# Kernel tuning notes

Hardware: AMD Instinct MI355X
Metric: run time of the kernel (lower is better)

The kernel has to match this reference:

```python
import jax, jax.numpy as jnp
import numpy as np


def rational_hat(points, centers, radius):
    # points: [B, P, 2], centers: [K, 2], radius: [1]
    # L1 distance of each point to each center: [B, P, K]
    norm = jnp.abs(points[:, :, None, :] - centers[None, None, :, :]).sum(-1)
    r = jnp.abs(radius[0])
    val = 1.0 / (1.0 + norm) - 1.0 / (1.0 + jnp.abs(r - norm))
    return val.sum(axis=1)  # [B, K]


def setup_inputs() -> dict:
    key = jax.random.key(0)
    k1, k2, k3, k4, k5 = jax.random.split(key, 5)
    B, N0, N1, N2, K = 32, 20000, 10000, 10000, 64
    return {
        "beta_0_up": jax.random.uniform(k1, (B, N0, 2), dtype=jnp.float32),
        "beta_0_down": jax.random.uniform(k2, (B, N0, 2), dtype=jnp.float32),
        "beta0_ext": jax.random.uniform(k3, (B, N1, 2), dtype=jnp.float32),
        "beta1_ext": jax.random.uniform(k4, (B, N2, 2), dtype=jnp.float32),
        "centers": jax.random.uniform(k5, (K, 2), dtype=jnp.float32),
        "radius": jnp.full((1,), 0.1, dtype=jnp.float32),
    }


def reference(beta_0_up, beta_0_down, beta0_ext, beta1_ext, centers, radius):
    x0, y0 = beta0_ext[..., 0], beta0_ext[..., 1]
    x1, y1 = beta1_ext[..., 0], beta1_ext[..., 1]
    b0_1st = jnp.stack([x0, 1.0 - x0], axis=-1)  # [B, N1, 2]
    b0_2nd = jnp.stack([y0, 1.0 - y0], axis=-1)
    b1_1st = jnp.stack([x1, 1.0 - x1], axis=-1)  # [B, N2, 2]
    b1_2nd = jnp.stack([y1, 1.0 - y1], axis=-1)
    ph_down = jnp.concatenate([beta_0_down, b0_1st, b1_1st], axis=1)  # [B, P, 2]
    ph_up = jnp.concatenate([beta_0_up, b0_2nd, b1_2nd], axis=1)
    up_out = rational_hat(ph_up, centers, radius)    # [B, K]
    down_out = rational_hat(ph_down, centers, radius)
    tpl = -((up_out - down_out) ** 2).sum()
    x = jnp.concatenate([up_out, down_out], axis=1)  # [B, 2K]
    return (x, tpl)
```

## Files before the change

kernel.cpp:

```cpp
#include <hip/hip_runtime.h>

#define NB 32
#define N0 20000
#define N1 10000
#define N2 10000
#define KC_A 8
#define KC_B 16
#define NBINS 4096
#define SENT 3.0e4f

__device__ __forceinline__ float sgpr(float x) {
    return __int_as_float(__builtin_amdgcn_readfirstlane(__float_as_int(x)));
}

__global__ __launch_bounds__(256, 8) void hat_kernel(
    const float* __restrict__ up0, const float* __restrict__ down0,
    const float* __restrict__ ext0, const float* __restrict__ ext1,
    const float* __restrict__ centers, const float* __restrict__ radius,
    float* __restrict__ out)
{
    const int tid  = threadIdx.x;
    const int lane = tid & 63;
    const int wave = tid >> 6;
    const float r  = sgpr(fabsf(radius[0]));
    const float nr = -r;

    __shared__ unsigned hist[NBINS];
    __shared__ float    red[4 * KC_B];

    if (blockIdx.x < 256) {
        const int id   = blockIdx.x;
        const int cc   = id & 3;
        const int side = (id >> 2) & 1;
        const int b    = id >> 3;
        const int cbase = cc * KC_B;

        for (int j = tid; j < NBINS; j += 256) hist[j] = 0;
        __syncthreads();

        const float2* e0 = (const float2*)(ext0 + (size_t)b * (N1*2));
        const float2* e1 = (const float2*)(ext1 + (size_t)b * (N2*2));
        for (int i = tid; i < N1; i += 256) {
            const float2 q0 = e0[i];
            const float2 q1 = e1[i];
            const float vv0 = (side == 0) ? q0.y : q0.x;
            const float vv1 = (side == 0) ? q1.y : q1.x;
            int b0 = (int)(vv0 * (float)NBINS);
            int b1 = (int)(vv1 * (float)NBINS);
            b0 = min(max(b0, 0), NBINS - 1);
            b1 = min(max(b1, 0), NBINS - 1);
            atomicAdd(&hist[b0], 1u);
            atomicAdd(&hist[b1], 1u);
        }
        __syncthreads();

        float Ak[KC_B], mk[KC_B];
        #pragma unroll
        for (int k = 0; k < KC_B; ++k) {
            const float cx = centers[2*(cbase+k)];
            const float cy = centers[2*(cbase+k)+1];
            Ak[k] = sgpr(fabsf(1.0f - (cx + cy)));
            mk[k] = sgpr(0.5f * (1.0f + (cx - cy)));
        }

        float part[KC_B];
        #pragma unroll
        for (int k = 0; k < KC_B; ++k) part[k] = 0.f;

        #pragma unroll
        for (int jj = 0; jj < NBINS/256; ++jj) {
            const int j = jj*256 + tid;
            const float cntf = (float)hist[j];
            const float vvj  = ((float)j + 0.5f) * (1.0f/(float)NBINS);
            #pragma unroll
            for (int k = 0; k < KC_B; ++k) {
                const float s  = vvj - mk[k];
                const float tt = fmaxf(Ak[k], 2.0f*fabsf(s));
                const float d1 = 1.0f + tt;
                const float rn = r - tt;
                const float d2 = 1.0f + fabsf(rn);
                const float rc = __builtin_amdgcn_rcpf(d1 * d2);
                part[k] = fmaf(cntf * (d2 - d1), rc, part[k]);
            }
        }

        {
            #pragma unroll
            for (int k = 0; k < 8; ++k) {
                const bool hi = lane & 32;
                const float send = hi ? part[k]   : part[k+8];
                const float keep = hi ? part[k+8] : part[k];
                part[k] = keep + __shfl_xor(send, 32, 64);
            }
            #pragma unroll
            for (int k = 0; k < 4; ++k) {
                const bool hi = lane & 16;
                const float send = hi ? part[k]   : part[k+4];
                const float keep = hi ? part[k+4] : part[k];
                part[k] = keep + __shfl_xor(send, 16, 64);
            }
            #pragma unroll
            for (int k = 0; k < 2; ++k) {
                const bool hi = lane & 8;
                const float send = hi ? part[k]   : part[k+2];
                const float keep = hi ? part[k+2] : part[k];
                part[k] = keep + __shfl_xor(send, 8, 64);
            }
            {
                const bool hi = lane & 4;
                const float send = hi ? part[0] : part[1];
                const float keep = hi ? part[1] : part[0];
                part[0] = keep + __shfl_xor(send, 4, 64);
            }
            part[0] += __shfl_xor(part[0], 2, 64);
            part[0] += __shfl_xor(part[0], 1, 64);
        }
        if ((lane & 3) == 0) red[wave * KC_B + (lane >> 2)] = part[0];
        __syncthreads();
        if (tid < KC_B) {
            const float s = red[tid] + red[KC_B + tid] + red[2*KC_B + tid] + red[3*KC_B + tid];
            atomicAdd(&out[b*128 + side*64 + cbase + tid], s);
        }
    } else {
        const int bid    = blockIdx.x - 256;
        const int tchunk = bid & 3;
        const int cc     = (bid >> 2) & 7;
        const int side   = (bid >> 5) & 1;
        const int b      = bid >> 6;
        const int cbase  = cc * KC_A;

        float uc[KC_A], vc[KC_A];
        #pragma unroll
        for (int k = 0; k < KC_A; ++k) {
            const float cx = centers[2*(cbase+k)];
            const float cy = centers[2*(cbase+k)+1];
            uc[k] = sgpr(cx + cy);
            vc[k] = sgpr(cx - cy);
        }

        const float4* base0 = (const float4*)((side == 0 ? up0 : down0) + (size_t)b * (N0*2));

        float acc[KC_A];
        #pragma unroll
        for (int k = 0; k < KC_A; ++k) acc[k] = 0.f;

        for (int t = tchunk*4 + wave; t < 79; t += 16) {
            const int i0 = t*128 + lane;
            const int i1 = i0 + 64;
            float u[4], v[4];
            if (i0 < 10000) {
                const float4 q = base0[i0];
                u[0] = q.x + q.y;  v[0] = q.x - q.y;
                u[1] = q.z + q.w;  v[1] = q.z - q.w;
            } else {
                u[0] = SENT; v[0] = 0.f; u[1] = SENT; v[1] = 0.f;
            }
            if (i1 < 10000) {
                const float4 q = base0[i1];
                u[2] = q.x + q.y;  v[2] = q.x - q.y;
                u[3] = q.z + q.w;  v[3] = q.z - q.w;
            } else {
                u[2] = SENT; v[2] = 0.f; u[3] = SENT; v[3] = 0.f;
            }

            #pragma unroll
            for (int k = 0; k < KC_A; ++k) {
                float dd[4], nm[4];
                #pragma unroll
                for (int p = 0; p < 4; ++p) {
                    const float du = u[p] - uc[k];
                    const float dv = v[p] - vc[k];
                    const float tt = fmaxf(fabsf(du), fabsf(dv));
                    const float d1 = 1.0f + tt;
                    const float n_ = fmaxf(fmaf(-2.0f, tt, r), nr);
                    nm[p] = n_;
                    dd[p] = d1 * (d1 + n_);
                }
                float s01 = nm[0] * dd[1];  s01 = fmaf(nm[1], dd[0], s01);
                float s23 = nm[2] * dd[3];  s23 = fmaf(nm[3], dd[2], s23);
                const float dd01 = dd[0] * dd[1];
                const float dd23 = dd[2] * dd[3];
                float S = s01 * dd23;       S = fmaf(s23, dd01, S);
                const float rc = __builtin_amdgcn_rcpf(dd01 * dd23);
                acc[k] = fmaf(S, rc, acc[k]);
            }
        }

        float a1[KC_A];
        #pragma unroll
        for (int k = 0; k < KC_A; ++k) a1[k] = acc[k];
        {
            #pragma unroll
            for (int k = 0; k < 4; ++k) {
                const bool hi = lane & 32;
                const float send = hi ? a1[k]   : a1[k+4];
                const float keep = hi ? a1[k+4] : a1[k];
                a1[k] = keep + __shfl_xor(send, 32, 64);
            }
            #pragma unroll
            for (int k = 0; k < 2; ++k) {
                const bool hi = lane & 16;
                const float send = hi ? a1[k]   : a1[k+2];
                const float keep = hi ? a1[k+2] : a1[k];
                a1[k] = keep + __shfl_xor(send, 16, 64);
            }
            {
                const bool hi = lane & 8;
                const float send = hi ? a1[0] : a1[1];
                const float keep = hi ? a1[1] : a1[0];
                a1[0] = keep + __shfl_xor(send, 8, 64);
            }
            a1[0] += __shfl_xor(a1[0], 4, 64);
            a1[0] += __shfl_xor(a1[0], 2, 64);
            a1[0] += __shfl_xor(a1[0], 1, 64);
        }
        if ((lane & 7) == 0) red[wave * KC_A + (lane >> 3)] = a1[0];
        __syncthreads();
        if (tid < KC_A) {
            const float s = red[tid] + red[KC_A + tid] + red[2*KC_A + tid] + red[3*KC_A + tid];
            atomicAdd(&out[b*128 + side*64 + cbase + tid], s);
        }
    }
}

__global__ __launch_bounds__(256) void tpl_kernel(float* __restrict__ out)
{
    __shared__ float red[256];
    float s = 0.f;
    for (int i = threadIdx.x; i < NB*64; i += 256) {
        const int b = i >> 6, k = i & 63;
        const float d = out[b*128 + k] - out[b*128 + 64 + k];
        s = fmaf(d, d, s);
    }
    red[threadIdx.x] = s;
    __syncthreads();
    for (int w = 128; w > 0; w >>= 1) {
        if (threadIdx.x < w) red[threadIdx.x] += red[threadIdx.x + w];
        __syncthreads();
    }
    if (threadIdx.x == 0) out[NB*128] = -red[0];
}

extern "C" void kernel_launch(void* const* d_in, const int* in_sizes, int n_in,
                              void* d_out, int out_size, void* d_ws, size_t ws_size,
                              hipStream_t stream) {
    const float* up0     = (const float*)d_in[0];
    const float* down0   = (const float*)d_in[1];
    const float* ext0    = (const float*)d_in[2];
    const float* ext1    = (const float*)d_in[3];
    const float* centers = (const float*)d_in[4];
    const float* radius  = (const float*)d_in[5];
    float* out = (float*)d_out;

    hipMemsetAsync(out, 0, NB * 128 * sizeof(float), stream);

    hat_kernel<<<dim3(256 + 2048), dim3(256), 0, stream>>>(
        up0, down0, ext0, ext1, centers, radius, out);
    tpl_kernel<<<1, 256, 0, stream>>>(out);
}
```

Before: 109.6 us.

## Widen dense-path center tiles and fold tpl reduction into last block

The dense branch now processes 16 centers per block instead of 8. Work is repartitioned into 28 blocks per (batch, side), 7 point chunks by 4 center groups, so each loaded point is reused across more centers and the grid totals 2048 blocks. The separate tpl_kernel launch is removed: every block increments a counter stored in the tpl output slot, and the last block to finish computes the squared-difference reduction. The risks are higher register pressure under launch_bounds(256,8) and reliance on threadfence ordering for the last-block pattern.

After: 155.1 us. 41.5% more time.

```diff
diff --git a/kernel.cpp b/kernel.cpp
--- a/kernel.cpp
+++ b/kernel.cpp
@@ -4,9 +4,10 @@
 #define N0 20000
 #define N1 10000
 #define N2 10000
-#define KC_A 8
+#define KC_A 16
 #define KC_B 16
 #define NBINS 4096
+#define NBLK_TOTAL 2048
 #define SENT 3.0e4f
 
 __device__ __forceinline__ float sgpr(float x) {
@@ -27,6 +28,7 @@
 
     __shared__ unsigned hist[NBINS];
     __shared__ float    red[4 * KC_B];
+    __shared__ int      is_last;
 
     if (blockIdx.x < 256) {
         const int id   = blockIdx.x;
@@ -122,12 +124,14 @@
             atomicAdd(&out[b*128 + side*64 + cbase + tid], s);
         }
     } else {
-        const int bid    = blockIdx.x - 256;
-        const int tchunk = bid & 3;
-        const int cc     = (bid >> 2) & 7;
-        const int side   = (bid >> 5) & 1;
-        const int b      = bid >> 6;
-        const int cbase  = cc * KC_A;
+        const int bid2 = blockIdx.x - 256;
+        const int bs   = bid2 / 28;
+        const int rem  = bid2 - bs * 28;
+        const int tch  = rem >> 2;
+        const int cc   = rem & 3;
+        const int side = bs & 1;
+        const int b    = bs >> 1;
+        const int cbase = cc * KC_A;
 
         float uc[KC_A], vc[KC_A];
         #pragma unroll
@@ -144,7 +148,7 @@
         #pragma unroll
         for (int k = 0; k < KC_A; ++k) acc[k] = 0.f;
 
-        for (int t = tchunk*4 + wave; t < 79; t += 16) {
+        for (int t = tch*4 + wave; t < 79; t += 28) {
             const int i0 = t*128 + lane;
             const int i1 = i0 + 64;
             float u[4], v[4];
@@ -186,59 +190,74 @@
             }
         }
 
-        float a1[KC_A];
-        #pragma unroll
-        for (int k = 0; k < KC_A; ++k) a1[k] = acc[k];
         {
             #pragma unroll
+            for (int k = 0; k < 8; ++k) {
+                const bool hi = lane & 32;
+                const float send = hi ? acc[k]   : acc[k+8];
+                const float keep = hi ? acc[k+8] : acc[k];
+                acc[k] = keep + __shfl_xor(send, 32, 64);
+            }
+            #pragma unroll
             for (int k = 0; k < 4; ++k) {
-                const bool hi = lane & 32;
-                const float send = hi ? a1[k]   : a1[k+4];
-                const float keep = hi ? a1[k+4] : a1[k];
-                a1[k] = keep + __shfl_xor(send, 32, 64);
+                const bool hi = lane & 16;
+                const float send = hi ? acc[k]   : acc[k+4];
+                const float keep = hi ? acc[k+4] : acc[k];
+                acc[k] = keep + __shfl_xor(send, 16, 64);
             }
             #pragma unroll
             for (int k = 0; k < 2; ++k) {
-                const bool hi = lane & 16;
-                const float send = hi ? a1[k]   : a1[k+2];
-                const float keep = hi ? a1[k+2] : a1[k];
-                a1[k] = keep + __shfl_xor(send, 16, 64);
+                const bool hi = lane & 8;
+                const float send = hi ? acc[k]   : acc[k+2];
+                const float keep = hi ? acc[k+2] : acc[k];
+                acc[k] = keep + __shfl_xor(send, 8, 64);
             }
             {
-                const bool hi = lane & 8;
-                const float send = hi ? a1[0] : a1[1];
-                const float keep = hi ? a1[1] : a1[0];
-                a1[0] = keep + __shfl_xor(send, 8, 64);
-            }
-            a1[0] += __shfl_xor(a1[0], 4, 64);
-            a1[0] += __shfl_xor(a1[0], 2, 64);
-            a1[0] += __shfl_xor(a1[0], 1, 64);
-        }
-        if ((lane & 7) == 0) red[wave * KC_A + (lane >> 3)] = a1[0];
+                const bool hi = lane & 4;
+                const float send = hi ? acc[0] : acc[1];
+                const float keep = hi ? acc[1] : acc[0];
+                acc[0] = keep + __shfl_xor(send, 4, 64);
+            }
+            acc[0] += __shfl_xor(acc[0], 2, 64);
+            acc[0] += __shfl_xor(acc[0], 1, 64);
+        }
+        if ((lane & 3) == 0) red[wave * KC_A + (lane >> 2)] = acc[0];
         __syncthreads();
         if (tid < KC_A) {
             const float s = red[tid] + red[KC_A + tid] + red[2*KC_A + tid] + red[3*KC_A + tid];
             atomicAdd(&out[b*128 + side*64 + cbase + tid], s);
         }
     }
-}
-
-__global__ __launch_bounds__(256) void tpl_kernel(float* __restrict__ out)
-{
-    __shared__ float red[256];
-    float s = 0.f;
-    for (int i = threadIdx.x; i < NB*64; i += 256) {
-        const int b = i >> 6, k = i & 63;
-        const float d = out[b*128 + k] - out[b*128 + 64 + k];
-        s = fmaf(d, d, s);
+
+    __syncthreads();
+    if (tid == 0) {
+        __threadfence();
+        const int old = atomicAdd((int*)&out[NB*128], 1);
+        is_last = (old == NBLK_TOTAL - 1);
     }
-    red[threadIdx.x] = s;
     __syncthreads();
-    for (int w = 128; w > 0; w >>= 1) {
-        if (threadIdx.x < w) red[threadIdx.x] += red[threadIdx.x + w];
-        __syncthreads();
+    if (is_last) {
+        if (tid == 0) __threadfence();
+        __syncthreads();
+        float s = 0.f;
+        for (int i = tid; i < NB*64; i += 256) {
+            const int bb = i >> 6, k = i & 63;
+            const float d = out[bb*128 + k] - out[bb*128 + 64 + k];
+            s = fmaf(d, d, s);
+        }
+        s += __shfl_xor(s, 32, 64);
+        s += __shfl_xor(s, 16, 64);
+        s += __shfl_xor(s, 8, 64);
+        s += __shfl_xor(s, 4, 64);
+        s += __shfl_xor(s, 2, 64);
+        s += __shfl_xor(s, 1, 64);
+        if (lane == 0) red[wave] = s;
+        __syncthreads();
+        if (tid == 0) {
+            const float tot = (red[0] + red[1]) + (red[2] + red[3]);
+            out[NB*128] = -tot;
+        }
     }
-    if (threadIdx.x == 0) out[NB*128] = -red[0];
 }
 
 extern "C" void kernel_launch(void* const* d_in, const int* in_sizes, int n_in,
@@ -252,9 +271,8 @@
     const float* radius  = (const float*)d_in[5];
     float* out = (float*)d_out;
 
-    hipMemsetAsync(out, 0, NB * 128 * sizeof(float), stream);
-
-    hat_kernel<<<dim3(256 + 2048), dim3(256), 0, stream>>>(
+    hipMemsetAsync(out, 0, (NB * 128 + 1) * sizeof(float), stream);
+
+    hat_kernel<<<dim3(NBLK_TOTAL), dim3(256), 0, stream>>>(
         up0, down0, ext0, ext1, centers, radius, out);
-    tpl_kernel<<<1, 256, 0, stream>>>(out);
 }
```
